# Kernel tuning notes

Hardware: AMD Instinct MI355X
Metric: run time of the kernel (lower is better)

The kernel has to match this reference:

```python
import jax, jax.numpy as jnp
import numpy as np

# constants from data_utils / args in the original repo
MPP0 = 0.2              # meter_per_pixel at process resolution
PROC_SIDE = 512.0       # process_satmap_sidelength
CAM_HEIGHT = 1.65       # camera height in meters
SHIFT_LON = 20.0        # args.shift_range_lon
SHIFT_LAT = 20.0        # args.shift_range_lat
ROT_RANGE = 10.0        # args.rotation_range (degrees)
ORI_H, ORI_W = 256, 1024  # original ground image size


def _bilinear_sample(img, uv):
    """Custom grid_sample: uv are absolute pixel coords (x,y), zero padding,
    returns (sampled [B,C,A,A], in-bounds mask [B,1,A,A])."""
    B, C, IH, IW = img.shape
    A1, A2 = uv.shape[1], uv.shape[2]
    ix, iy = uv[..., 0], uv[..., 1]
    x0 = jnp.floor(ix); y0 = jnp.floor(iy)
    x1 = x0 + 1.0;      y1 = y0 + 1.0
    w00 = (x1 - ix) * (y1 - iy)
    w01 = (ix - x0) * (y1 - iy)
    w10 = (x1 - ix) * (iy - y0)
    w11 = (ix - x0) * (iy - y0)
    valid = (ix >= 0) & (ix <= IW - 1) & (iy >= 0) & (iy <= IH - 1)
    x0c = jnp.clip(x0, 0, IW - 1).astype(jnp.int32)
    x1c = jnp.clip(x1, 0, IW - 1).astype(jnp.int32)
    y0c = jnp.clip(y0, 0, IH - 1).astype(jnp.int32)
    y1c = jnp.clip(y1, 0, IH - 1).astype(jnp.int32)
    flat = img.reshape(B, C, IH * IW)

    def gather(yy, xx):
        idx = (yy * IW + xx).reshape(B, 1, A1 * A2)
        v = jnp.take_along_axis(flat, jnp.broadcast_to(idx, (B, C, A1 * A2)), axis=2)
        return v.reshape(B, C, A1, A2)

    out = (gather(y0c, x0c) * w00[:, None]
           + gather(y0c, x1c) * w01[:, None]
           + gather(y1c, x0c) * w10[:, None]
           + gather(y1c, x1c) * w11[:, None])
    out = out * valid[:, None].astype(img.dtype)
    return out, valid[:, None]


def _sat2world(A, B, predict_height=None, dtype=jnp.float32):
    """sat pixel grid -> world XYZ1 homogeneous coords [B,A,A,4]."""
    r = jnp.arange(A, dtype=dtype)
    hh, ww = jnp.meshgrid(r, r, indexing='ij')  # hh: row index, ww: col index
    c = float(A // 2)
    mpp = MPP0 * PROC_SIDE / A
    # Aff_sat2real = mpp * [[0,1],[1,0]] applied to uv_center where uv=[w,h]
    X = jnp.broadcast_to(mpp * (hh - c), (B, A, A))
    Z = jnp.broadcast_to(mpp * (ww - c), (B, A, A))
    if predict_height is None:
        Y = jnp.zeros((B, A, A), dtype)
    else:
        Y = -predict_height[:, 0]  # [B,A,A]
    ones = jnp.ones((B, A, A), dtype)
    return jnp.stack([X, Y, Z, ones], axis=-1)


def _world2grd_uv(shift_u, shift_v, heading, XYZ1, camera_k, H, W):
    """Project world points into ground-image pixel coords. Returns (uv [B,A,A,2], depth mask [B,A,A,1])."""
    B = heading.shape[0]
    su = SHIFT_LON * shift_u[:, 0]
    sv = SHIFT_LAT * shift_v[:, 0]
    h = heading[:, 0] * (ROT_RANGE / 180.0) * jnp.pi
    cos = jnp.cos(-h); sin = jnp.sin(-h)
    z = jnp.zeros_like(cos); o = jnp.ones_like(cos)
    R = jnp.stack([cos, z, -sin, z, o, z, sin, z, cos], axis=-1).reshape(B, 3, 3)
    T = jnp.stack([sv, CAM_HEIGHT * o, -su], axis=-1)[..., None]  # [B,3,1]
    K = camera_k
    K = K.at[:, 0, :].multiply(W / ORI_W).at[:, 1, :].multiply(H / ORI_H)
    P = K @ jnp.concatenate([R, T], axis=-1)  # [B,3,4]
    uv1 = jnp.einsum('bij,bhwj->bhwi', P, XYZ1)  # [B,A,A,3]
    d = jnp.maximum(uv1[..., 2:], 1e-6)
    uv = uv1[..., :2] / d
    mask = uv1[..., 2:] > 1e-6
    return uv, mask


def setup_inputs() -> dict:
    key = jax.random.key(0)
    ks = jax.random.split(key, 6)
    B, C, H, W, A = 32, 256, 32, 128, 64
    grd_f = jax.random.normal(ks[0], (B, C, H, W), dtype=jnp.float32)
    predict_height = jax.random.uniform(ks[1], (B, 1, A, A), dtype=jnp.float32) * 2.0
    shift_u = (jax.random.uniform(ks[2], (B, 1), dtype=jnp.float32) * 2.0 - 1.0)
    shift_v = (jax.random.uniform(ks[3], (B, 1), dtype=jnp.float32) * 2.0 - 1.0)
    heading = (jax.random.uniform(ks[4], (B, 1), dtype=jnp.float32) * 2.0 - 1.0)
    fx = fy = 500.0
    K = jnp.array([[fx, 0.0, ORI_W / 2.0], [0.0, fy, ORI_H / 2.0], [0.0, 0.0, 1.0]], dtype=jnp.float32)
    camera_k = jnp.broadcast_to(K, (B, 3, 3)).copy()
    sat_embedding = jax.random.uniform(ks[5], (1, C, A, A), dtype=jnp.float32)
    return {"grd_f": grd_f, "predict_height": predict_height, "shift_u": shift_u,
            "shift_v": shift_v, "heading": heading, "camera_k": camera_k,
            "sat_embedding": sat_embedding}


def reference(grd_f, predict_height, shift_u, shift_v, heading, camera_k, sat_embedding):
    B, C, H, W = grd_f.shape
    A = sat_embedding.shape[-1]
    # project_sat_original: flat-ground (Y=0) projection
    XYZ_flat = _sat2world(A, B, None, grd_f.dtype)
    uv0, mask1 = _world2grd_uv(shift_u, shift_v, heading, XYZ_flat, camera_k, H, W)
    grd_orig, mask2 = _bilinear_sample(grd_f, uv0)
    # project_grd_to_map: height-aware projection
    XYZ_h = _sat2world(A, B, predict_height, grd_f.dtype)
    uv_h, _ = _world2grd_uv(shift_u, shift_v, heading, XYZ_h, camera_k, H, W)
    grd_h, _ = _bilinear_sample(grd_f, uv_h)
    # learned gate blend (as in inverse_map)
    out = grd_h * sat_embedding + grd_orig * (1.0 - sat_embedding)
    return out
```

## Files before the change

kernel.cpp:

```cpp
#include <hip/hip_runtime.h>
#include <math.h>

namespace {
constexpr int B_ = 32, C_ = 256, H_ = 32, W_ = 128, A_ = 64;
constexpr int AA = A_ * A_;
constexpr int HW = H_ * W_;
constexpr int NPOS = B_ * AA;
constexpr int CPB = 8;
constexpr int TPB = 1024;
constexpr float MPP = 1.6f;
constexpr float PI_F = 3.14159265358979323846f;
typedef float vf4 __attribute__((ext_vector_type(4)));
}

struct Pmat {
    float p00, p01, p02, p03;
    float p10, p11, p12, p13;
    float p20, p21, p22, p23;
};

__device__ __forceinline__ Pmat make_P(int b,
                                       const float* __restrict__ shift_u,
                                       const float* __restrict__ shift_v,
                                       const float* __restrict__ heading,
                                       const float* __restrict__ camk) {
    float su = 20.f * shift_u[b];
    float sv = 20.f * shift_v[b];
    float h  = heading[b] * (10.f / 180.f) * PI_F;
    float ch = cosf(h);
    float sh = -sinf(h);

    const float* K = camk + b * 9;
    float k00 = K[0] * 0.125f, k01 = K[1] * 0.125f, k02 = K[2] * 0.125f;
    float k10 = K[3] * 0.125f, k11 = K[4] * 0.125f, k12 = K[5] * 0.125f;
    float k20 = K[6],          k21 = K[7],          k22 = K[8];

    Pmat P;
    P.p00 = k00 * ch + k02 * sh;  P.p01 = k01;
    P.p02 = -k00 * sh + k02 * ch; P.p03 = k00 * sv + k01 * 1.65f - k02 * su;
    P.p10 = k10 * ch + k12 * sh;  P.p11 = k11;
    P.p12 = -k10 * sh + k12 * ch; P.p13 = k10 * sv + k11 * 1.65f - k12 * su;
    P.p20 = k20 * ch + k22 * sh;  P.p21 = k21;
    P.p22 = -k20 * sh + k22 * ch; P.p23 = k20 * sv + k21 * 1.65f - k22 * su;
    return P;
}

__device__ __forceinline__ float4 uv_at(const Pmat& P, int pos, float Y) {
    int i = pos >> 6, j = pos & 63;
    float X = MPP * (float)(i - 32);
    float Z = MPP * (float)(j - 32);

    float u1 = P.p00 * X + P.p02 * Z + P.p03;
    float v1 = P.p10 * X + P.p12 * Z + P.p13;
    float w1 = P.p20 * X + P.p22 * Z + P.p23;

    float d0 = fmaxf(w1, 1e-6f);
    float u0 = u1 / d0, v0 = v1 / d0;

    float u1h = u1 + P.p01 * Y;
    float v1h = v1 + P.p11 * Y;
    float w1h = w1 + P.p21 * Y;
    float dh = fmaxf(w1h, 1e-6f);
    float uh = u1h / dh, vh = v1h / dh;

    return make_float4(u0, v0, uh, vh);
}

__global__ __launch_bounds__(256) void uv_kernel(
        const float* __restrict__ ph,
        const float* __restrict__ shift_u,
        const float* __restrict__ shift_v,
        const float* __restrict__ heading,
        const float* __restrict__ camk,
        float4* __restrict__ uvout) {
    int gid = blockIdx.x * 256 + threadIdx.x;
    if (gid >= NPOS) return;
    int b = gid >> 12;
    int pos = gid & (AA - 1);
    Pmat P = make_P(b, shift_u, shift_v, heading, camk);
    uvout[gid] = uv_at(P, pos, -ph[gid]);
}

__device__ __forceinline__ void mk(float ix, float iy, float4& w, int& ad) {
    bool valid = (ix >= 0.f) && (ix <= (float)(W_ - 1)) &&
                 (iy >= 0.f) && (iy <= (float)(H_ - 1));
    float x0f = floorf(ix), y0f = floorf(iy);
    float fx = ix - x0f, fy = iy - y0f;
    float xa = fminf(fmaxf(x0f, 0.f), 127.f);
    float ya = fminf(fmaxf(y0f, 0.f), 31.f);
    int a = (int)fmaf(ya, 128.f, xa);
    float gx = 1.f - fx, gy = 1.f - fy;
    w = valid ? make_float4(gx * gy, fx * gy, gx * fy, fx * fy)
              : make_float4(0.f, 0.f, 0.f, 0.f);
    ad = valid ? a : 0;
}

__device__ __forceinline__ float tap4(const float* __restrict__ im, int ad, float4 w) {
    const float* t = im + ad;
    return fmaf(w.x, t[0], fmaf(w.y, t[1], fmaf(w.z, t[128], w.w * t[129])));
}

template <bool PRECOMP>
__global__ __launch_bounds__(TPB) void proj_kernel(
        const float* __restrict__ grd,
        const float4* __restrict__ uv,
        const float* __restrict__ sat,
        float* __restrict__ out,
        const float* __restrict__ ph,
        const float* __restrict__ shift_u,
        const float* __restrict__ shift_v,
        const float* __restrict__ heading,
        const float* __restrict__ camk) {
    __shared__ float img[2 * HW + 132];
    int cg = blockIdx.x, b = blockIdx.y;
    int c0 = cg * CPB;
    int tid = threadIdx.x;
    int p0 = tid * 4;
    int bbase = b << 12;

    const float* gbase = grd + ((size_t)b * C_ + c0) * HW;

    float4 streg = ((const float4*)gbase)[tid];

    if (tid < 33) {
        ((float4*)(img + HW))[tid] = make_float4(0.f, 0.f, 0.f, 0.f);
        ((float4*)(img + 2 * HW))[tid] = make_float4(0.f, 0.f, 0.f, 0.f);
    }

    float4 w[4][2];
    int ad[4][2];
    if (PRECOMP) {
        const float4* uvb = uv + bbase;
#pragma unroll
        for (int k = 0; k < 4; ++k) {
            float4 q = uvb[p0 + k];
            mk(q.x, q.y, w[k][0], ad[k][0]);
            mk(q.z, q.w, w[k][1], ad[k][1]);
        }
    } else {
        Pmat P = make_P(b, shift_u, shift_v, heading, camk);
        const float* phb = ph + bbase;
#pragma unroll
        for (int k = 0; k < 4; ++k) {
            float4 q = uv_at(P, p0 + k, -phb[p0 + k]);
            mk(q.x, q.y, w[k][0], ad[k][0]);
            mk(q.z, q.w, w[k][1], ad[k][1]);
        }
    }

    float* outbase = out + ((size_t)b * C_ + c0) * AA + p0;
    const float* satbase = sat + (size_t)c0 * AA + p0;

#pragma unroll
    for (int cp = 0; cp < CPB; ++cp) {
        int bufo = (cp & 1) * HW;
        *(float4*)(img + bufo + p0) = streg;
        float4 nxt;
        if (cp + 1 < CPB)
            nxt = ((const float4*)(gbase + (size_t)(cp + 1) * HW))[tid];
        float4 sv = *(const float4*)(satbase + (size_t)cp * AA);
        asm volatile("s_waitcnt lgkmcnt(0)" ::: "memory");
        __builtin_amdgcn_s_barrier();

        const float* im = img + bufo;
        float r[4];
#pragma unroll
        for (int k = 0; k < 4; ++k) {
            float g0 = tap4(im, ad[k][0], w[k][0]);
            float gh = tap4(im, ad[k][1], w[k][1]);
            float s = (k == 0) ? sv.x : (k == 1) ? sv.y : (k == 2) ? sv.z : sv.w;
            r[k] = fmaf(s, gh - g0, g0);
        }
        vf4 rv = {r[0], r[1], r[2], r[3]};
        __builtin_nontemporal_store(rv, (vf4*)(outbase + (size_t)cp * AA));
        streg = nxt;

    }
}

extern "C" void kernel_launch(void* const* d_in, const int* in_sizes, int n_in,
                              void* d_out, int out_size, void* d_ws, size_t ws_size,
                              hipStream_t stream) {
    (void)in_sizes; (void)n_in; (void)out_size;
    const float* grd  = (const float*)d_in[0];
    const float* ph   = (const float*)d_in[1];
    const float* s_u  = (const float*)d_in[2];
    const float* s_v  = (const float*)d_in[3];
    const float* hd   = (const float*)d_in[4];
    const float* ck   = (const float*)d_in[5];
    const float* sat  = (const float*)d_in[6];
    float* out = (float*)d_out;

    const size_t uv_bytes = (size_t)NPOS * sizeof(float4);
    if (ws_size >= uv_bytes) {
        float4* uvws = (float4*)d_ws;
        uv_kernel<<<(NPOS + 255) / 256, 256, 0, stream>>>(ph, s_u, s_v, hd, ck, uvws);
        proj_kernel<true><<<dim3(C_ / CPB, B_), TPB, 0, stream>>>(
            grd, uvws, sat, out, ph, s_u, s_v, hd, ck);
    } else {
        proj_kernel<false><<<dim3(C_ / CPB, B_), TPB, 0, stream>>>(
            grd, nullptr, sat, out, ph, s_u, s_v, hd, ck);
    }
}
```

Measured before the change: 54.96 us.

## Load all channel planes into shared memory upfront, drop per-channel barriers

Halves channels per block to four and stages all four ground-feature planes in shared memory with a single barrier. This replaces the double-buffered per-channel load, wait and barrier loop. The loads are issued before the UV/weight computation so their latency overlaps that math. In exchange the grid doubles, the UV/weight setup is repeated for twice as many blocks, and each block uses more LDS.

```diff
diff --git a/kernel.cpp b/kernel.cpp
--- a/kernel.cpp
+++ b/kernel.cpp
@@ -6,7 +6,7 @@
 constexpr int AA = A_ * A_;
 constexpr int HW = H_ * W_;
 constexpr int NPOS = B_ * AA;
-constexpr int CPB = 8;
+constexpr int CPB = 4;
 constexpr int TPB = 1024;
 constexpr float MPP = 1.6f;
 constexpr float PI_F = 3.14159265358979323846f;
@@ -101,7 +101,7 @@
 }
 
 template <bool PRECOMP>
-__global__ __launch_bounds__(TPB) void proj_kernel(
+__global__ __launch_bounds__(TPB, 8) void proj_kernel(
         const float* __restrict__ grd,
         const float4* __restrict__ uv,
         const float* __restrict__ sat,
@@ -111,21 +111,22 @@
         const float* __restrict__ shift_v,
         const float* __restrict__ heading,
         const float* __restrict__ camk) {
-    __shared__ float img[2 * HW + 132];
+    __shared__ float img[CPB * HW + 132];
     int cg = blockIdx.x, b = blockIdx.y;
     int c0 = cg * CPB;
     int tid = threadIdx.x;
     int p0 = tid * 4;
     int bbase = b << 12;
 
-    const float* gbase = grd + ((size_t)b * C_ + c0) * HW;
-
-    float4 streg = ((const float4*)gbase)[tid];
-
-    if (tid < 33) {
-        ((float4*)(img + HW))[tid] = make_float4(0.f, 0.f, 0.f, 0.f);
-        ((float4*)(img + 2 * HW))[tid] = make_float4(0.f, 0.f, 0.f, 0.f);
-    }
+    const float4* gbase = (const float4*)(grd + ((size_t)b * C_ + c0) * HW);
+
+    float4 s0 = gbase[tid];
+    float4 s1 = gbase[HW / 4 + tid];
+    float4 s2 = gbase[2 * (HW / 4) + tid];
+    float4 s3 = gbase[3 * (HW / 4) + tid];
+
+    if (tid < 33)
+        ((float4*)(img + CPB * HW))[tid] = make_float4(0.f, 0.f, 0.f, 0.f);
 
     float4 w[4][2];
     int ad[4][2];
@@ -148,21 +149,19 @@
         }
     }
 
+    ((float4*)img)[tid] = s0;
+    ((float4*)img)[HW / 4 + tid] = s1;
+    ((float4*)img)[2 * (HW / 4) + tid] = s2;
+    ((float4*)img)[3 * (HW / 4) + tid] = s3;
+    __syncthreads();
+
     float* outbase = out + ((size_t)b * C_ + c0) * AA + p0;
     const float* satbase = sat + (size_t)c0 * AA + p0;
 
 #pragma unroll
-    for (int cp = 0; cp < CPB; ++cp) {
-        int bufo = (cp & 1) * HW;
-        *(float4*)(img + bufo + p0) = streg;
-        float4 nxt;
-        if (cp + 1 < CPB)
-            nxt = ((const float4*)(gbase + (size_t)(cp + 1) * HW))[tid];
-        float4 sv = *(const float4*)(satbase + (size_t)cp * AA);
-        asm volatile("s_waitcnt lgkmcnt(0)" ::: "memory");
-        __builtin_amdgcn_s_barrier();
-
-        const float* im = img + bufo;
+    for (int c = 0; c < CPB; ++c) {
+        const float* im = img + c * HW;
+        float4 sv = *(const float4*)(satbase + (size_t)c * AA);
         float r[4];
 #pragma unroll
         for (int k = 0; k < 4; ++k) {
@@ -172,9 +171,7 @@
             r[k] = fmaf(s, gh - g0, g0);
         }
         vf4 rv = {r[0], r[1], r[2], r[3]};
-        __builtin_nontemporal_store(rv, (vf4*)(outbase + (size_t)cp * AA));
-        streg = nxt;
-
+        __builtin_nontemporal_store(rv, (vf4*)(outbase + (size_t)c * AA));
     }
 }
 
```

Result: slower. 77.47 us (+40.9%).
